# Performance work log

Hardware: AMD Instinct MI355X
Metric: run time of the kernel (lower is better)

Reference implementation:

```python
import jax, jax.numpy as jnp
import numpy as np

N_EMBD = 1024
N_HEAD = 16
D_K = N_EMBD // N_HEAD


def setup_inputs() -> dict:
    key = jax.random.key(0)
    ks = jax.random.split(key, 9)
    B, L, D = 4, 2048, N_EMBD
    s = 1.0 / np.sqrt(D)
    inp = {
        "x": jax.random.normal(ks[0], (B, L, D), dtype=jnp.float32),
        "mask": jnp.tril(jnp.ones((1, 1, L, L), dtype=jnp.int32)),
        "Wq": jax.random.uniform(ks[1], (D, D), jnp.float32, -s, s),
        "bq": jax.random.uniform(ks[2], (D,), jnp.float32, -s, s),
        "Wk": jax.random.uniform(ks[3], (D, D), jnp.float32, -s, s),
        "bk": jax.random.uniform(ks[4], (D,), jnp.float32, -s, s),
        "Wv": jax.random.uniform(ks[5], (D, D), jnp.float32, -s, s),
        "bv": jax.random.uniform(ks[6], (D,), jnp.float32, -s, s),
        "Wo": jax.random.uniform(ks[7], (D, D), jnp.float32, -s, s),
        "bo": jax.random.uniform(ks[8], (D,), jnp.float32, -s, s),
    }
    return inp


def reference(x, mask, Wq, bq, Wk, bk, Wv, bv, Wo, bo):
    B, L, D = x.shape
    H, dk = N_HEAD, D_K
    # torch nn.Linear: y = x @ W.T + b
    def proj(W, b):
        y = jnp.einsum('bld,ed->ble', x, W) + b
        return y.reshape(B, L, H, dk).transpose(0, 2, 1, 3)  # [B,H,L,dk]
    q = proj(Wq, bq)
    k = proj(Wk, bk)
    v = proj(Wv, bv)
    scores = jnp.einsum('bhqd,bhkd->bhqk', q, k) / jnp.sqrt(jnp.float32(dk))
    scores = jnp.where(mask == 0, -jnp.inf, scores)
    attn_weights = jax.nn.softmax(scores, axis=-1)  # [B,H,L,L]
    out = jnp.einsum('bhqk,bhkd->bhqd', attn_weights, v)
    out = out.transpose(0, 2, 1, 3).reshape(B, L, D)
    out = jnp.einsum('bld,ed->ble', out, Wo) + bo
    return out, attn_weights
```

## Files before the change

### kernel.cpp

```cpp
#include <hip/hip_runtime.h>
#include <stdint.h>


typedef __attribute__((ext_vector_type(8))) __bf16 bf16x8;
typedef __attribute__((ext_vector_type(4))) float f32x4;

__device__ inline unsigned short f2b(float f) {
  union { float f; unsigned int i; } v; v.f = f;
  unsigned int i = v.i;
  return (unsigned short)((i + 0x7fffu + ((i >> 16) & 1u)) >> 16);
}

__device__ inline f32x4 mfma16(bf16x8 a, bf16x8 b, f32x4 c) {
  return __builtin_amdgcn_mfma_f32_16x16x32_bf16(a, b, c, 0, 0, 0);
}

#define GLD16(gp, lp) __builtin_amdgcn_global_load_lds( \
    (const __attribute__((address_space(1))) void*)(gp), \
    (__attribute__((address_space(3))) void*)(lp), 16, 0, 0)

#define VMWAIT(n) asm volatile("s_waitcnt vmcnt(" #n ")" ::: "memory")
#define LGKM0()   asm volatile("s_waitcnt lgkmcnt(0)" ::: "memory")
#define BAR()     do { asm volatile("" ::: "memory"); \
                       __builtin_amdgcn_s_barrier(); \
                       asm volatile("" ::: "memory"); } while (0)

__global__ __launch_bounds__(256) void f2b_kernel(
    const float* __restrict__ src, unsigned short* __restrict__ dst, int n8)
{
  int i = blockIdx.x * 256 + threadIdx.x;
  if (i >= n8) return;
  const float4* s = (const float4*)src;
  float4 a = s[2 * i], b = s[2 * i + 1];
  unsigned short o[8] __attribute__((aligned(16)));
  o[0] = f2b(a.x); o[1] = f2b(a.y); o[2] = f2b(a.z); o[3] = f2b(a.w);
  o[4] = f2b(b.x); o[5] = f2b(b.y); o[6] = f2b(b.z); o[7] = f2b(b.w);
  *(uint4*)(dst + (size_t)i * 8) = *(const uint4*)o;
}

template <bool OUTF32>
__global__ __launch_bounds__(256) void gemm_bt(
    const unsigned short* __restrict__ A, const unsigned short* __restrict__ B,
    const float* __restrict__ bias, void* __restrict__ Cv,
    int M, int N, int K)
{
  __shared__ unsigned short As[128 * 64];
  __shared__ unsigned short Bs[128 * 64];
  const int tid  = threadIdx.x;
  const int w    = tid >> 6;
  const int lane = tid & 63;
  const int ln   = lane & 15;
  const int quad = lane >> 4;
  const int m0 = blockIdx.x * 128;
  const int n0 = blockIdx.y * 128;
  const int wr = (w >> 1) * 64;
  const int wc = (w & 1) * 64;

  f32x4 acc[4][4];
#pragma unroll
  for (int r = 0; r < 4; ++r)
#pragma unroll
    for (int c = 0; c < 4; ++c) acc[r][c] = (f32x4){0.f, 0.f, 0.f, 0.f};

  for (int kb = 0; kb < K; kb += 64) {
#pragma unroll
    for (int i = 0; i < 4; ++i) {
      int ci  = i * 256 + tid;
      int row = ci >> 3;
      int co  = (ci & 7) * 8;
      GLD16(A + (size_t)(m0 + row) * K + kb + co, &As[(i * 256 + w * 64) * 8]);
      GLD16(B + (size_t)(n0 + row) * K + kb + co, &Bs[(i * 256 + w * 64) * 8]);
    }
    __syncthreads();
#pragma unroll
    for (int ks = 0; ks < 2; ++ks) {
      bf16x8 af[4], bfr[4];
#pragma unroll
      for (int r = 0; r < 4; ++r)
        af[r] = *(const bf16x8*)&As[(wr + r * 16 + ln) * 64 + ks * 32 + quad * 8];
#pragma unroll
      for (int c = 0; c < 4; ++c)
        bfr[c] = *(const bf16x8*)&Bs[(wc + c * 16 + ln) * 64 + ks * 32 + quad * 8];
#pragma unroll
      for (int r = 0; r < 4; ++r)
#pragma unroll
        for (int c = 0; c < 4; ++c)
          acc[r][c] = mfma16(af[r], bfr[c], acc[r][c]);
    }
    __syncthreads();
  }
#pragma unroll
  for (int c = 0; c < 4; ++c) {
    int j = n0 + wc + c * 16 + ln;
    float bj = bias[j];
#pragma unroll
    for (int r = 0; r < 4; ++r)
#pragma unroll
      for (int e = 0; e < 4; ++e) {
        int row = m0 + wr + r * 16 + quad * 4 + e;
        float v = acc[r][c][e] + bj;
        if (OUTF32) ((float*)Cv)[(size_t)row * N + j] = v;
        else ((unsigned short*)Cv)[(size_t)row * N + j] = f2b(v);
      }
  }
}

__global__ __launch_bounds__(256) void transpose_v(
    const unsigned short* __restrict__ V, unsigned short* __restrict__ Vt)
{
  __shared__ unsigned short T[64][72];
  const int tid = threadIdx.x;
  const int lt  = blockIdx.x;
  const int bh  = blockIdx.y;
  const int b = bh >> 4, h = bh & 15;
  const int l0 = lt * 64;
#pragma unroll
  for (int i = 0; i < 2; ++i) {
    int ci = i * 256 + tid;
    int row = ci >> 3;
    int co  = (ci & 7) * 8;
    uint4 v = *(const uint4*)(V + (size_t)(b * 2048 + l0 + row) * 1024 + h * 64 + co);
    *(uint4*)&T[row][co] = v;
  }
  __syncthreads();
  const int d   = tid >> 2;
  const int seg = tid & 3;
  unsigned short tmp[16] __attribute__((aligned(16)));
#pragma unroll
  for (int j = 0; j < 16; ++j) tmp[j] = T[seg * 16 + j][d];
  size_t dst = ((size_t)bh * 64 + d) * 2048 + l0 + seg * 16;
  *(uint4*)(Vt + dst)     = *(const uint4*)tmp;
  *(uint4*)(Vt + dst + 8) = *(const uint4*)(tmp + 8);
}

__device__ __forceinline__ void stage64x64_swz(
    const unsigned short* __restrict__ g, int gstride,
    unsigned short* lds, int tid, int w)
{
#pragma unroll
  for (int i = 0; i < 2; ++i) {
    int ci  = i * 256 + tid;
    int row = ci >> 3;
    int c   = (ci & 7) ^ (row & 7);
    GLD16(g + (size_t)row * gstride + c * 8, lds + (i * 256 + w * 64) * 8);
  }
}

__global__ __launch_bounds__(256, 4) void attn_kernel(
    const unsigned short* __restrict__ Q, const unsigned short* __restrict__ Kg,
    const unsigned short* __restrict__ Vt, float* __restrict__ attnw,
    unsigned short* __restrict__ O)
{
  __shared__ unsigned short Ks[2][64 * 64];
  __shared__ unsigned short Vs[64 * 64];
  __shared__ float Psf[64 * 64];

  const int tid  = threadIdx.x;
  const int w    = tid >> 6;
  const int lane = tid & 63;
  const int ln   = lane & 15;
  const int quad = lane >> 4;
  const int bh = blockIdx.y;
  const int b = bh >> 4, h = bh & 15;
  const size_t head_off = (size_t)b * 2048 * 1024 + (size_t)h * 64;

#pragma unroll 1
  for (int qi = 0; qi < 2; ++qi) {
    const int qt   = qi ? (31 - (int)blockIdx.x) : (int)blockIdx.x;
    const int q0   = qt * 64;
    const int nkt  = qt + 1;
    const int qrow = q0 + w * 16 + quad * 4;

    unsigned short* Qst = (unsigned short*)Psf;
    stage64x64_swz(Q + head_off + (size_t)q0 * 1024, 1024, Qst, tid, w);
    VMWAIT(0); BAR();
    bf16x8 qf0, qf1;
    {
      int row = w * 16 + ln, r7 = row & 7;
      qf0 = *(const bf16x8*)&Qst[row * 64 + ((quad    ) ^ r7) * 8];
      qf1 = *(const bf16x8*)&Qst[row * 64 + (((quad + 4) ^ r7)) * 8];
    }

    float lsum[4] = {0.f, 0.f, 0.f, 0.f};
    stage64x64_swz(Kg + head_off, 1024, &Ks[0][0], tid, w);
    VMWAIT(0); BAR();
    int cur = 0;
    for (int kt = 0; kt < nkt; ++kt) {
      if (kt + 1 < nkt)
        stage64x64_swz(Kg + head_off + (size_t)(kt + 1) * 64 * 1024, 1024,
                       &Ks[cur ^ 1][0], tid, w);
#pragma unroll
      for (int t = 0; t < 4; ++t) {
        int row = t * 16 + ln, r7 = row & 7;
        bf16x8 kf0 = *(const bf16x8*)&Ks[cur][row * 64 + ((quad    ) ^ r7) * 8];
        bf16x8 kf1 = *(const bf16x8*)&Ks[cur][row * 64 + (((quad + 4) ^ r7)) * 8];
        f32x4 s = mfma16(qf0, kf0, (f32x4){0.f, 0.f, 0.f, 0.f});
        s = mfma16(qf1, kf1, s);
        int kidx = kt * 64 + row;
#pragma unroll
        for (int r = 0; r < 4; ++r)
          lsum[r] += (kidx <= qrow + r) ? __expf(s[r] * 0.125f) : 0.f;
      }
      if (kt + 1 < nkt) VMWAIT(0);
      BAR();
      cur ^= 1;
    }
    float rl[4];
#pragma unroll
    for (int r = 0; r < 4; ++r) {
      float v = lsum[r];
      v += __shfl_xor(v, 1); v += __shfl_xor(v, 2);
      v += __shfl_xor(v, 4); v += __shfl_xor(v, 8);
      rl[r] = 1.f / v;
    }

    f32x4 accO[4];
#pragma unroll
    for (int dt = 0; dt < 4; ++dt) accO[dt] = (f32x4){0.f, 0.f, 0.f, 0.f};
    stage64x64_swz(Kg + head_off, 1024, &Ks[0][0], tid, w);
    VMWAIT(0); BAR();
    cur = 0;
    for (int kt = 0; kt < nkt; ++kt) {
      const int pre = (kt + 1 < nkt);
      stage64x64_swz(Vt + (size_t)(bh * 64) * 2048 + kt * 64, 2048, Vs, tid, w);
      if (pre)
        stage64x64_swz(Kg + head_off + (size_t)(kt + 1) * 64 * 1024, 1024,
                       &Ks[cur ^ 1][0], tid, w);
#pragma unroll
      for (int t = 0; t < 4; ++t) {
        int row = t * 16 + ln, r7 = row & 7;
        bf16x8 kf0 = *(const bf16x8*)&Ks[cur][row * 64 + ((quad    ) ^ r7) * 8];
        bf16x8 kf1 = *(const bf16x8*)&Ks[cur][row * 64 + (((quad + 4) ^ r7)) * 8];
        f32x4 s = mfma16(qf0, kf0, (f32x4){0.f, 0.f, 0.f, 0.f});
        s = mfma16(qf1, kf1, s);
        int kidx = kt * 64 + row;
#pragma unroll
        for (int r = 0; r < 4; ++r) {
          float p = (kidx <= qrow + r) ? __expf(s[r] * 0.125f) * rl[r] : 0.f;
          int prow = w * 16 + quad * 4 + r;
          int pc   = t * 16 + ln;
          Psf[prow * 64 + ((((pc >> 2) ^ (prow & 15)) << 2) | (pc & 3))] = p;
        }
      }
      if (pre) { VMWAIT(2); } else { VMWAIT(0); }
      LGKM0();
      BAR();
      bf16x8 pfr0, pfr1;
      {
        int prl = w * 16 + ln, rx = prl & 15;
        const float* Pr = &Psf[prl * 64];
        float4 a0 = *(const float4*)&Pr[((2 * quad    ) ^ rx) * 4];
        float4 a1 = *(const float4*)&Pr[((2 * quad + 1) ^ rx) * 4];
        float4 b0 = *(const float4*)&Pr[((8 + 2 * quad) ^ rx) * 4];
        float4 b1 = *(const float4*)&Pr[((9 + 2 * quad) ^ rx) * 4];
        unsigned short t0[8] __attribute__((aligned(16)));
        unsigned short t1[8] __attribute__((aligned(16)));
        t0[0]=f2b(a0.x); t0[1]=f2b(a0.y); t0[2]=f2b(a0.z); t0[3]=f2b(a0.w);
        t0[4]=f2b(a1.x); t0[5]=f2b(a1.y); t0[6]=f2b(a1.z); t0[7]=f2b(a1.w);
        t1[0]=f2b(b0.x); t1[1]=f2b(b0.y); t1[2]=f2b(b0.z); t1[3]=f2b(b0.w);
        t1[4]=f2b(b1.x); t1[5]=f2b(b1.y); t1[6]=f2b(b1.z); t1[7]=f2b(b1.w);
        pfr0 = *(const bf16x8*)t0;
        pfr1 = *(const bf16x8*)t1;
      }
#pragma unroll
      for (int dt = 0; dt < 4; ++dt) {
        int row = dt * 16 + ln, r7 = row & 7;
        bf16x8 vf0 = *(const bf16x8*)&Vs[row * 64 + ((quad    ) ^ r7) * 8];
        bf16x8 vf1 = *(const bf16x8*)&Vs[row * 64 + (((quad + 4) ^ r7)) * 8];
        accO[dt] = mfma16(pfr0, vf0, accO[dt]);
        accO[dt] = mfma16(pfr1, vf1, accO[dt]);
      }
      {
        int srow = w * 16 + (lane >> 2);
        int seg  = lane & 3;
        int rx   = srow & 15;
        const float* Pr = &Psf[srow * 64];
        float4 o0 = *(const float4*)&Pr[((4 * seg    ) ^ rx) * 4];
        float4 o1 = *(const float4*)&Pr[((4 * seg + 1) ^ rx) * 4];
        float4 o2 = *(const float4*)&Pr[((4 * seg + 2) ^ rx) * 4];
        float4 o3 = *(const float4*)&Pr[((4 * seg + 3) ^ rx) * 4];
        float* dst = attnw + ((size_t)bh * 2048 + (size_t)(q0 + srow)) * 2048
                   + kt * 64 + seg * 16;
        ((float4*)dst)[0] = o0; ((float4*)dst)[1] = o1;
        ((float4*)dst)[2] = o2; ((float4*)dst)[3] = o3;
      }
      VMWAIT(4);
      LGKM0();
      BAR();
      cur ^= 1;
    }
    {
      int row = tid >> 2, seg = tid & 3;
      float4 z = make_float4(0.f, 0.f, 0.f, 0.f);
      for (int kt = nkt; kt < 32; ++kt) {
        float* dst = attnw + ((size_t)bh * 2048 + (size_t)(q0 + row)) * 2048
                   + kt * 64 + seg * 16;
        ((float4*)dst)[0] = z; ((float4*)dst)[1] = z;
        ((float4*)dst)[2] = z; ((float4*)dst)[3] = z;
      }
    }
#pragma unroll
    for (int dt = 0; dt < 4; ++dt)
#pragma unroll
      for (int e = 0; e < 4; ++e) {
        int row = w * 16 + quad * 4 + e;
        int col = h * 64 + dt * 16 + ln;
        O[(size_t)(b * 2048 + q0 + row) * 1024 + col] = f2b(accO[dt][e]);
      }
  }
}

extern "C" void kernel_launch(void* const* d_in, const int* in_sizes, int n_in,
                              void* d_out, int out_size, void* d_ws, size_t ws_size,
                              hipStream_t stream) {
  const float* x  = (const float*)d_in[0];
  const float* Wq = (const float*)d_in[2];
  const float* bq = (const float*)d_in[3];
  const float* Wk = (const float*)d_in[4];
  const float* bk = (const float*)d_in[5];
  const float* Wv = (const float*)d_in[6];
  const float* bv = (const float*)d_in[7];
  const float* Wo = (const float*)d_in[8];
  const float* bo = (const float*)d_in[9];

  float* out   = (float*)d_out;
  float* attnw = out + (size_t)8192 * 1024;

  const size_t NE = (size_t)8192 * 1024;
  const size_t WE = (size_t)1024 * 1024;
  unsigned short* xb  = (unsigned short*)d_ws;
  unsigned short* Wqb = xb + NE;
  unsigned short* Wkb = Wqb + WE;
  unsigned short* Wvb = Wkb + WE;
  unsigned short* Wob = Wvb + WE;
  unsigned short* Qb  = Wob + WE;
  unsigned short* Kb  = Qb + NE;
  unsigned short* Vb  = Kb + NE;
  unsigned short* Vtb = xb;
  unsigned short* Ob  = Vb;

  dim3 gb(256);
  f2b_kernel<<<dim3((NE / 8 + 255) / 256), gb, 0, stream>>>(x, xb, (int)(NE / 8));
  f2b_kernel<<<dim3((WE / 8 + 255) / 256), gb, 0, stream>>>(Wq, Wqb, (int)(WE / 8));
  f2b_kernel<<<dim3((WE / 8 + 255) / 256), gb, 0, stream>>>(Wk, Wkb, (int)(WE / 8));
  f2b_kernel<<<dim3((WE / 8 + 255) / 256), gb, 0, stream>>>(Wv, Wvb, (int)(WE / 8));
  f2b_kernel<<<dim3((WE / 8 + 255) / 256), gb, 0, stream>>>(Wo, Wob, (int)(WE / 8));

  dim3 gg(64, 8);
  gemm_bt<false><<<gg, gb, 0, stream>>>(xb, Wqb, bq, Qb, 8192, 1024, 1024);
  gemm_bt<false><<<gg, gb, 0, stream>>>(xb, Wkb, bk, Kb, 8192, 1024, 1024);
  gemm_bt<false><<<gg, gb, 0, stream>>>(xb, Wvb, bv, Vb, 8192, 1024, 1024);
  transpose_v<<<dim3(32, 64), gb, 0, stream>>>(Vb, Vtb);
  attn_kernel<<<dim3(16, 64), gb, 0, stream>>>(Qb, Kb, Vtb, attnw, Ob);
  gemm_bt<true><<<gg, gb, 0, stream>>>(Ob, Wob, bo, out, 8192, 1024, 1024);
}
```

Baseline: 1.853 ms.

## Fuse QKV GEMM, split row-sum pass, shuffle P to registers

Merges the three Q/K/V projection GEMMs into one launch by treating the concatenated weights as a single 3072-wide matrix, which assumes Wq/Wk/Wv sit contiguously in the workspace. The softmax denominator moves to a separate kernel over lower-triangular tile pairs that accumulates with atomics into a buffer held in the output region. The attention kernel then makes one pass, double-buffers V, and builds the bf16 P operand with cross-lane shuffles instead of round-tripping through shared memory, writing attention weights straight from registers. The costs are atomics, an extra zeroing launch, recomputing QK^T in two kernels, and reusing the output buffer as scratch.

```diff
diff --git a/kernel.cpp b/kernel.cpp
--- a/kernel.cpp
+++ b/kernel.cpp
@@ -4,6 +4,7 @@
 
 typedef __attribute__((ext_vector_type(8))) __bf16 bf16x8;
 typedef __attribute__((ext_vector_type(4))) float f32x4;
+typedef unsigned int uint;
 
 __device__ inline unsigned short f2b(float f) {
   union { float f; unsigned int i; } v; v.f = f;
@@ -20,7 +21,6 @@
     (__attribute__((address_space(3))) void*)(lp), 16, 0, 0)
 
 #define VMWAIT(n) asm volatile("s_waitcnt vmcnt(" #n ")" ::: "memory")
-#define LGKM0()   asm volatile("s_waitcnt lgkmcnt(0)" ::: "memory")
 #define BAR()     do { asm volatile("" ::: "memory"); \
                        __builtin_amdgcn_s_barrier(); \
                        asm volatile("" ::: "memory"); } while (0)
@@ -36,6 +36,11 @@
   o[0] = f2b(a.x); o[1] = f2b(a.y); o[2] = f2b(a.z); o[3] = f2b(a.w);
   o[4] = f2b(b.x); o[5] = f2b(b.y); o[6] = f2b(b.z); o[7] = f2b(b.w);
   *(uint4*)(dst + (size_t)i * 8) = *(const uint4*)o;
+}
+
+__global__ __launch_bounds__(256) void zero_f32(float* __restrict__ p, int n) {
+  int i = blockIdx.x * 256 + threadIdx.x;
+  if (i < n) p[i] = 0.f;
 }
 
 template <bool OUTF32>
@@ -105,6 +110,76 @@
   }
 }
 
+__global__ __launch_bounds__(256) void gemm_qkv(
+    const unsigned short* __restrict__ A, const unsigned short* __restrict__ W,
+    const float* __restrict__ bq, const float* __restrict__ bk,
+    const float* __restrict__ bv, unsigned short* __restrict__ Qo,
+    unsigned short* __restrict__ Ko, unsigned short* __restrict__ Vo)
+{
+  const int K = 1024;
+  __shared__ unsigned short As[128 * 64];
+  __shared__ unsigned short Bs[128 * 64];
+  const int tid  = threadIdx.x;
+  const int w    = tid >> 6;
+  const int lane = tid & 63;
+  const int ln   = lane & 15;
+  const int quad = lane >> 4;
+  const int m0 = blockIdx.x * 128;
+  const int n0 = blockIdx.y * 128;
+  const int wr = (w >> 1) * 64;
+  const int wc = (w & 1) * 64;
+
+  f32x4 acc[4][4];
+#pragma unroll
+  for (int r = 0; r < 4; ++r)
+#pragma unroll
+    for (int c = 0; c < 4; ++c) acc[r][c] = (f32x4){0.f, 0.f, 0.f, 0.f};
+
+  for (int kb = 0; kb < K; kb += 64) {
+#pragma unroll
+    for (int i = 0; i < 4; ++i) {
+      int ci  = i * 256 + tid;
+      int row = ci >> 3;
+      int co  = (ci & 7) * 8;
+      GLD16(A + (size_t)(m0 + row) * K + kb + co, &As[(i * 256 + w * 64) * 8]);
+      GLD16(W + (size_t)(n0 + row) * K + kb + co, &Bs[(i * 256 + w * 64) * 8]);
+    }
+    __syncthreads();
+#pragma unroll
+    for (int ks = 0; ks < 2; ++ks) {
+      bf16x8 af[4], bfr[4];
+#pragma unroll
+      for (int r = 0; r < 4; ++r)
+        af[r] = *(const bf16x8*)&As[(wr + r * 16 + ln) * 64 + ks * 32 + quad * 8];
+#pragma unroll
+      for (int c = 0; c < 4; ++c)
+        bfr[c] = *(const bf16x8*)&Bs[(wc + c * 16 + ln) * 64 + ks * 32 + quad * 8];
+#pragma unroll
+      for (int r = 0; r < 4; ++r)
+#pragma unroll
+        for (int c = 0; c < 4; ++c)
+          acc[r][c] = mfma16(af[r], bfr[c], acc[r][c]);
+    }
+    __syncthreads();
+  }
+#pragma unroll
+  for (int c = 0; c < 4; ++c) {
+    int j   = n0 + wc + c * 16 + ln;
+    int sel = j >> 10;
+    int jc  = j & 1023;
+    const float* bp = (sel == 0) ? bq : (sel == 1) ? bk : bv;
+    unsigned short* op = (sel == 0) ? Qo : (sel == 1) ? Ko : Vo;
+    float bj = bp[jc];
+#pragma unroll
+    for (int r = 0; r < 4; ++r)
+#pragma unroll
+      for (int e = 0; e < 4; ++e) {
+        int row = m0 + wr + r * 16 + quad * 4 + e;
+        op[(size_t)row * 1024 + jc] = f2b(acc[r][c][e] + bj);
+      }
+  }
+}
+
 __global__ __launch_bounds__(256) void transpose_v(
     const unsigned short* __restrict__ V, unsigned short* __restrict__ Vt)
 {
@@ -146,15 +221,64 @@
   }
 }
 
+__global__ __launch_bounds__(256) void lsum_kernel(
+    const unsigned short* __restrict__ Q, const unsigned short* __restrict__ Kg,
+    float* __restrict__ lsum)
+{
+  __shared__ unsigned short Qs[64 * 64];
+  __shared__ unsigned short Ks[64 * 64];
+  const int tid  = threadIdx.x;
+  const int w    = tid >> 6;
+  const int lane = tid & 63;
+  const int ln   = lane & 15;
+  const int quad = lane >> 4;
+  const int idx = blockIdx.x;
+  const int bh  = blockIdx.y;
+  const int b = bh >> 4, h = bh & 15;
+  int qt = (int)((sqrtf(8.f * (float)idx + 1.f) - 1.f) * 0.5f);
+  while ((qt + 1) * (qt + 2) / 2 <= idx) ++qt;
+  while (qt * (qt + 1) / 2 > idx) --qt;
+  const int kt = idx - qt * (qt + 1) / 2;
+  const size_t head_off = (size_t)b * 2048 * 1024 + (size_t)h * 64;
+
+  stage64x64_swz(Q  + head_off + (size_t)qt * 64 * 1024, 1024, Qs, tid, w);
+  stage64x64_swz(Kg + head_off + (size_t)kt * 64 * 1024, 1024, Ks, tid, w);
+  VMWAIT(0); BAR();
+
+  bf16x8 qf0, qf1;
+  {
+    int row = w * 16 + ln, r7 = row & 7;
+    qf0 = *(const bf16x8*)&Qs[row * 64 + ((quad    ) ^ r7) * 8];
+    qf1 = *(const bf16x8*)&Qs[row * 64 + ((quad + 4) ^ r7) * 8];
+  }
+  const int qidx = qt * 64 + w * 16 + ln;
+  float acc = 0.f;
+#pragma unroll
+  for (int t = 0; t < 4; ++t) {
+    int row = t * 16 + ln, r7 = row & 7;
+    bf16x8 kf0 = *(const bf16x8*)&Ks[row * 64 + ((quad    ) ^ r7) * 8];
+    bf16x8 kf1 = *(const bf16x8*)&Ks[row * 64 + ((quad + 4) ^ r7) * 8];
+    f32x4 s = mfma16(kf0, qf0, (f32x4){0.f, 0.f, 0.f, 0.f});
+    s = mfma16(kf1, qf1, s);
+    int kbase = kt * 64 + t * 16 + quad * 4;
+#pragma unroll
+    for (int e = 0; e < 4; ++e)
+      acc += (kbase + e <= qidx) ? __expf(s[e] * 0.125f) : 0.f;
+  }
+  acc += __shfl_xor(acc, 16, 64);
+  acc += __shfl_xor(acc, 32, 64);
+  if (lane < 16)
+    atomicAdd(&lsum[(size_t)bh * 2048 + qidx], acc);
+}
+
 __global__ __launch_bounds__(256, 4) void attn_kernel(
     const unsigned short* __restrict__ Q, const unsigned short* __restrict__ Kg,
-    const unsigned short* __restrict__ Vt, float* __restrict__ attnw,
-    unsigned short* __restrict__ O)
-{
+    const unsigned short* __restrict__ Vt, const float* __restrict__ lsum,
+    float* __restrict__ attnw, unsigned short* __restrict__ O)
+{
+  __shared__ unsigned short Qs[64 * 64];
   __shared__ unsigned short Ks[2][64 * 64];
-  __shared__ unsigned short Vs[64 * 64];
-  __shared__ float Psf[64 * 64];
-
+  __shared__ unsigned short Vs[2][64 * 64];
   const int tid  = threadIdx.x;
   const int w    = tid >> 6;
   const int lane = tid & 63;
@@ -163,130 +287,100 @@
   const int bh = blockIdx.y;
   const int b = bh >> 4, h = bh & 15;
   const size_t head_off = (size_t)b * 2048 * 1024 + (size_t)h * 64;
+  const int src0 = ln + ((quad & 1) << 5);
+  const int src1 = src0 + 16;
+  const bool hi2 = (quad >> 1) & 1;
 
 #pragma unroll 1
   for (int qi = 0; qi < 2; ++qi) {
     const int qt   = qi ? (31 - (int)blockIdx.x) : (int)blockIdx.x;
     const int q0   = qt * 64;
     const int nkt  = qt + 1;
-    const int qrow = q0 + w * 16 + quad * 4;
-
-    unsigned short* Qst = (unsigned short*)Psf;
-    stage64x64_swz(Q + head_off + (size_t)q0 * 1024, 1024, Qst, tid, w);
+    const int qidx = q0 + w * 16 + ln;
+
+    stage64x64_swz(Q + head_off + (size_t)q0 * 1024, 1024, Qs, tid, w);
     VMWAIT(0); BAR();
     bf16x8 qf0, qf1;
     {
       int row = w * 16 + ln, r7 = row & 7;
-      qf0 = *(const bf16x8*)&Qst[row * 64 + ((quad    ) ^ r7) * 8];
-      qf1 = *(const bf16x8*)&Qst[row * 64 + (((quad + 4) ^ r7)) * 8];
-    }
-
-    float lsum[4] = {0.f, 0.f, 0.f, 0.f};
+      qf0 = *(const bf16x8*)&Qs[row * 64 + ((quad    ) ^ r7) * 8];
+      qf1 = *(const bf16x8*)&Qs[row * 64 + ((quad + 4) ^ r7) * 8];
+    }
+    const float rl = 1.f / lsum[(size_t)bh * 2048 + qidx];
+
+    f32x4 accO[4];
+#pragma unroll
+    for (int dt = 0; dt < 4; ++dt) accO[dt] = (f32x4){0.f, 0.f, 0.f, 0.f};
+
     stage64x64_swz(Kg + head_off, 1024, &Ks[0][0], tid, w);
+    stage64x64_swz(Vt + (size_t)bh * 64 * 2048, 2048, &Vs[0][0], tid, w);
     VMWAIT(0); BAR();
     int cur = 0;
     for (int kt = 0; kt < nkt; ++kt) {
-      if (kt + 1 < nkt)
+      const int pre = (kt + 1 < nkt);
+      if (pre) {
         stage64x64_swz(Kg + head_off + (size_t)(kt + 1) * 64 * 1024, 1024,
                        &Ks[cur ^ 1][0], tid, w);
+        stage64x64_swz(Vt + (size_t)bh * 64 * 2048 + (kt + 1) * 64, 2048,
+                       &Vs[cur ^ 1][0], tid, w);
+      }
+      float p[4][4];
 #pragma unroll
       for (int t = 0; t < 4; ++t) {
         int row = t * 16 + ln, r7 = row & 7;
         bf16x8 kf0 = *(const bf16x8*)&Ks[cur][row * 64 + ((quad    ) ^ r7) * 8];
-        bf16x8 kf1 = *(const bf16x8*)&Ks[cur][row * 64 + (((quad + 4) ^ r7)) * 8];
-        f32x4 s = mfma16(qf0, kf0, (f32x4){0.f, 0.f, 0.f, 0.f});
-        s = mfma16(qf1, kf1, s);
-        int kidx = kt * 64 + row;
-#pragma unroll
-        for (int r = 0; r < 4; ++r)
-          lsum[r] += (kidx <= qrow + r) ? __expf(s[r] * 0.125f) : 0.f;
-      }
-      if (kt + 1 < nkt) VMWAIT(0);
-      BAR();
-      cur ^= 1;
-    }
-    float rl[4];
-#pragma unroll
-    for (int r = 0; r < 4; ++r) {
-      float v = lsum[r];
-      v += __shfl_xor(v, 1); v += __shfl_xor(v, 2);
-      v += __shfl_xor(v, 4); v += __shfl_xor(v, 8);
-      rl[r] = 1.f / v;
-    }
-
-    f32x4 accO[4];
-#pragma unroll
-    for (int dt = 0; dt < 4; ++dt) accO[dt] = (f32x4){0.f, 0.f, 0.f, 0.f};
-    stage64x64_swz(Kg + head_off, 1024, &Ks[0][0], tid, w);
-    VMWAIT(0); BAR();
-    cur = 0;
-    for (int kt = 0; kt < nkt; ++kt) {
-      const int pre = (kt + 1 < nkt);
-      stage64x64_swz(Vt + (size_t)(bh * 64) * 2048 + kt * 64, 2048, Vs, tid, w);
-      if (pre)
-        stage64x64_swz(Kg + head_off + (size_t)(kt + 1) * 64 * 1024, 1024,
-                       &Ks[cur ^ 1][0], tid, w);
+        bf16x8 kf1 = *(const bf16x8*)&Ks[cur][row * 64 + ((quad + 4) ^ r7) * 8];
+        f32x4 s = mfma16(kf0, qf0, (f32x4){0.f, 0.f, 0.f, 0.f});
+        s = mfma16(kf1, qf1, s);
+        int kbase = kt * 64 + t * 16 + quad * 4;
+#pragma unroll
+        for (int e = 0; e < 4; ++e)
+          p[t][e] = (kbase + e <= qidx) ? __expf(s[e] * 0.125f) * rl : 0.f;
+      }
+      {
+        float* arow = attnw + ((size_t)bh * 2048 + (size_t)qidx) * 2048 + kt * 64;
+#pragma unroll
+        for (int t = 0; t < 4; ++t) {
+          float4 pv = make_float4(p[t][0], p[t][1], p[t][2], p[t][3]);
+          *(float4*)(arow + t * 16 + quad * 4) = pv;
+        }
+      }
+      uint dw[4][2];
 #pragma unroll
       for (int t = 0; t < 4; ++t) {
-        int row = t * 16 + ln, r7 = row & 7;
-        bf16x8 kf0 = *(const bf16x8*)&Ks[cur][row * 64 + ((quad    ) ^ r7) * 8];
-        bf16x8 kf1 = *(const bf16x8*)&Ks[cur][row * 64 + (((quad + 4) ^ r7)) * 8];
-        f32x4 s = mfma16(qf0, kf0, (f32x4){0.f, 0.f, 0.f, 0.f});
-        s = mfma16(qf1, kf1, s);
-        int kidx = kt * 64 + row;
-#pragma unroll
-        for (int r = 0; r < 4; ++r) {
-          float p = (kidx <= qrow + r) ? __expf(s[r] * 0.125f) * rl[r] : 0.f;
-          int prow = w * 16 + quad * 4 + r;
-          int pc   = t * 16 + ln;
-          Psf[prow * 64 + ((((pc >> 2) ^ (prow & 15)) << 2) | (pc & 3))] = p;
-        }
-      }
-      if (pre) { VMWAIT(2); } else { VMWAIT(0); }
-      LGKM0();
-      BAR();
-      bf16x8 pfr0, pfr1;
-      {
-        int prl = w * 16 + ln, rx = prl & 15;
-        const float* Pr = &Psf[prl * 64];
-        float4 a0 = *(const float4*)&Pr[((2 * quad    ) ^ rx) * 4];
-        float4 a1 = *(const float4*)&Pr[((2 * quad + 1) ^ rx) * 4];
-        float4 b0 = *(const float4*)&Pr[((8 + 2 * quad) ^ rx) * 4];
-        float4 b1 = *(const float4*)&Pr[((9 + 2 * quad) ^ rx) * 4];
-        unsigned short t0[8] __attribute__((aligned(16)));
-        unsigned short t1[8] __attribute__((aligned(16)));
-        t0[0]=f2b(a0.x); t0[1]=f2b(a0.y); t0[2]=f2b(a0.z); t0[3]=f2b(a0.w);
-        t0[4]=f2b(a1.x); t0[5]=f2b(a1.y); t0[6]=f2b(a1.z); t0[7]=f2b(a1.w);
-        t1[0]=f2b(b0.x); t1[1]=f2b(b0.y); t1[2]=f2b(b0.z); t1[3]=f2b(b0.w);
-        t1[4]=f2b(b1.x); t1[5]=f2b(b1.y); t1[6]=f2b(b1.z); t1[7]=f2b(b1.w);
-        pfr0 = *(const bf16x8*)t0;
-        pfr1 = *(const bf16x8*)t1;
+        dw[t][0] = (uint)f2b(p[t][0]) | ((uint)f2b(p[t][1]) << 16);
+        dw[t][1] = (uint)f2b(p[t][2]) | ((uint)f2b(p[t][3]) << 16);
+      }
+      bf16x8 pa[2];
+#pragma unroll
+      for (int ks = 0; ks < 2; ++ks) {
+        uint a0 = (uint)__shfl((int)dw[2 * ks][0],     src0, 64);
+        uint b0 = (uint)__shfl((int)dw[2 * ks + 1][0], src0, 64);
+        uint a1 = (uint)__shfl((int)dw[2 * ks][1],     src0, 64);
+        uint b1 = (uint)__shfl((int)dw[2 * ks + 1][1], src0, 64);
+        uint c0 = (uint)__shfl((int)dw[2 * ks][0],     src1, 64);
+        uint d0 = (uint)__shfl((int)dw[2 * ks + 1][0], src1, 64);
+        uint c1 = (uint)__shfl((int)dw[2 * ks][1],     src1, 64);
+        uint d1 = (uint)__shfl((int)dw[2 * ks + 1][1], src1, 64);
+        union { uint u[4]; bf16x8 v; } U;
+        U.u[0] = hi2 ? b0 : a0;
+        U.u[1] = hi2 ? b1 : a1;
+        U.u[2] = hi2 ? d0 : c0;
+        U.u[3] = hi2 ? d1 : c1;
+        pa[ks] = U.v;
       }
 #pragma unroll
       for (int dt = 0; dt < 4; ++dt) {
         int row = dt * 16 + ln, r7 = row & 7;
-        bf16x8 vf0 = *(const bf16x8*)&Vs[row * 64 + ((quad    ) ^ r7) * 8];
-        bf16x8 vf1 = *(const bf16x8*)&Vs[row * 64 + (((quad + 4) ^ r7)) * 8];
-        accO[dt] = mfma16(pfr0, vf0, accO[dt]);
-        accO[dt] = mfma16(pfr1, vf1, accO[dt]);
-      }
-      {
-        int srow = w * 16 + (lane >> 2);
-        int seg  = lane & 3;
-        int rx   = srow & 15;
-        const float* Pr = &Psf[srow * 64];
-        float4 o0 = *(const float4*)&Pr[((4 * seg    ) ^ rx) * 4];
-        float4 o1 = *(const float4*)&Pr[((4 * seg + 1) ^ rx) * 4];
-        float4 o2 = *(const float4*)&Pr[((4 * seg + 2) ^ rx) * 4];
-        float4 o3 = *(const float4*)&Pr[((4 * seg + 3) ^ rx) * 4];
-        float* dst = attnw + ((size_t)bh * 2048 + (size_t)(q0 + srow)) * 2048
-                   + kt * 64 + seg * 16;
-        ((float4*)dst)[0] = o0; ((float4*)dst)[1] = o1;
-        ((float4*)dst)[2] = o2; ((float4*)dst)[3] = o3;
-      }
-      VMWAIT(4);
-      LGKM0();
-      BAR();
+        bf16x8 vf0 = *(const bf16x8*)&Vs[cur][row * 64 + ((quad    ) ^ r7) * 8];
+        bf16x8 vf1 = *(const bf16x8*)&Vs[cur][row * 64 + ((quad + 4) ^ r7) * 8];
+        accO[dt] = mfma16(pa[0], vf0, accO[dt]);
+        accO[dt] = mfma16(pa[1], vf1, accO[dt]);
+      }
+      if (pre) {
+        VMWAIT(4);
+        BAR();
+      }
       cur ^= 1;
     }
     {
@@ -338,6 +432,7 @@
   unsigned short* Vb  = Kb + NE;
   unsigned short* Vtb = xb;
   unsigned short* Ob  = Vb;
+  float* lsum = out;
 
   dim3 gb(256);
   f2b_kernel<<<dim3((NE / 8 + 255) / 256), gb, 0, stream>>>(x, xb, (int)(NE / 8));
@@ -346,11 +441,10 @@
   f2b_kernel<<<dim3((WE / 8 + 255) / 256), gb, 0, stream>>>(Wv, Wvb, (int)(WE / 8));
   f2b_kernel<<<dim3((WE / 8 + 255) / 256), gb, 0, stream>>>(Wo, Wob, (int)(WE / 8));
 
-  dim3 gg(64, 8);
-  gemm_bt<false><<<gg, gb, 0, stream>>>(xb, Wqb, bq, Qb, 8192, 1024, 1024);
-  gemm_bt<false><<<gg, gb, 0, stream>>>(xb, Wkb, bk, Kb, 8192, 1024, 1024);
-  gemm_bt<false><<<gg, gb, 0, stream>>>(xb, Wvb, bv, Vb, 8192, 1024, 1024);
+  gemm_qkv<<<dim3(64, 24), gb, 0, stream>>>(xb, Wqb, bq, bk, bv, Qb, Kb, Vb);
   transpose_v<<<dim3(32, 64), gb, 0, stream>>>(Vb, Vtb);
-  attn_kernel<<<dim3(16, 64), gb, 0, stream>>>(Qb, Kb, Vtb, attnw, Ob);
-  gemm_bt<true><<<gg, gb, 0, stream>>>(Ob, Wob, bo, out, 8192, 1024, 1024);
-}
+  zero_f32<<<dim3(512), gb, 0, stream>>>(lsum, 64 * 2048);
+  lsum_kernel<<<dim3(528, 64), gb, 0, stream>>>(Qb, Kb, lsum);
+  attn_kernel<<<dim3(16, 64), gb, 0, stream>>>(Qb, Kb, Vtb, lsum, attnw, Ob);
+  gemm_bt<true><<<dim3(64, 8), gb, 0, stream>>>(Ob, Wob, bo, out, 8192, 1024, 1024);
+}
```

Result: faster. 1.762 ms (-4.9%).
